# Kernel tuning notes

Hardware: AMD Instinct MI355X
Metric: run time of the kernel (lower is better)

The kernel has to match this reference:

```python
import jax, jax.numpy as jnp
import numpy as np

D, N, F_IN, F_OUT = 2, 4096, 128, 128
DENSITY = 0.005  # avg degree ~20 per row in the 0/1 attention graphs
NEG_INF = -1e30


def setup_inputs() -> dict:
    key = jax.random.key(0)
    ks = jax.random.split(key, 12)
    X = jax.random.normal(ks[0], (D, N, F_IN), dtype=jnp.float32)
    # Dense Laplacian operator used in torch.sparse.mm(L[i], h_p); scaled so tanh stays non-degenerate
    L = jax.random.normal(ks[1], (D, N, N), dtype=jnp.float32) / np.float32(np.sqrt(N))
    # Upper/lower adjacency: 0/1 matrices (GATLayer extracts edges via adj == 1)
    L_u = (jax.random.uniform(ks[2], (D, N, N)) < DENSITY).astype(jnp.float32)
    L_d = (jax.random.uniform(ks[3], (D, N, N)) < DENSITY).astype(jnp.float32)
    s = np.float32(0.05)
    Wp = jax.random.normal(ks[4], (D, F_IN, F_OUT), dtype=jnp.float32) * s
    Ws = jax.random.normal(ks[5], (D, F_IN, F_OUT), dtype=jnp.float32) * s
    Wu = jax.random.normal(ks[6], (D, F_IN, F_OUT), dtype=jnp.float32) * s
    au1 = jax.random.normal(ks[7], (D, F_OUT), dtype=jnp.float32) * s
    au2 = jax.random.normal(ks[8], (D, F_OUT), dtype=jnp.float32) * s
    Wd = jax.random.normal(ks[9], (D, F_IN, F_OUT), dtype=jnp.float32) * s
    ad1 = jax.random.normal(ks[10], (D, F_OUT), dtype=jnp.float32) * s
    ad2 = jax.random.normal(ks[11], (D, F_OUT), dtype=jnp.float32) * s
    return {"X": X, "L": L, "L_u": L_u, "L_d": L_d,
            "Wp": Wp, "Ws": Ws, "Wu": Wu, "au1": au1, "au2": au2,
            "Wd": Wd, "ad1": ad1, "ad2": ad2, "dimensions": D}


def _gat(x, adj, W, a1, a2):
    # GATLayer.forward with boundary=False: linear -> edge scores -> LeakyReLU ->
    # row-wise softmax restricted to adj==1 entries -> sparse mm.
    h = x @ W                                   # [N, F_OUT]
    s1 = h @ a1                                 # [N]  (a_1 linear, bias=False)
    s2 = h @ a2                                 # [N]
    scores = jax.nn.leaky_relu(s1[:, None] + s2[None, :])  # [N, N], slope 0.01
    mask = adj == 1.0
    scores = jnp.where(mask, scores, NEG_INF)
    attn = jax.nn.softmax(scores, axis=1)
    attn = jnp.where(mask, attn, 0.0)           # zero rows with no edges (sparse softmax semantics)
    return attn @ h                             # [N, F_OUT]


def _san_dim(x, L, Lu, Ld, Wp, Ws, Wu, au1, au2, Wd, ad1, ad2):
    h_p = jnp.tanh(L @ (x @ Wp))
    h_s = jnp.tanh(x @ Ws)
    h_u = jnp.tanh(_gat(x, Lu, Wu, au1, au2))
    h_d = jnp.tanh(_gat(x, Ld, Wd, ad1, ad2))
    return h_s + h_u + h_d + h_p


def reference(X, L, L_u, L_d, Wp, Ws, Wu, au1, au2, Wd, ad1, ad2, dimensions):
    # vmap over the `dimensions` simplex levels (all per-level params stacked on axis 0)
    return jax.vmap(_san_dim)(X, L, L_u, L_d, Wp, Ws, Wu, au1, au2, Wd, ad1, ad2)
```

## Files before the change

### kernel.cpp

```cpp
#include <hip/hip_runtime.h>
#include <hip/hip_bf16.h>

#define NN 4096
#define FD 128
#define NDIM 2
#define CAP 256

#define OFF_HMAT 0
#define OFF_SVEC 3145728
#define OFF_HP   3178496
#define OFF_GU   7372800
#define OFF_GD   8421376
#define OFF_H0T  9469952

typedef _Float16 f16x8 __attribute__((ext_vector_type(8)));
typedef float f32x4 __attribute__((ext_vector_type(4)));

union P4 { _Float16 h[4]; int2 i2; };

__device__ __forceinline__ float f4get(const float4& v, int j) {
    return j == 0 ? v.x : j == 1 ? v.y : j == 2 ? v.z : v.w;
}

__global__ __launch_bounds__(256) void k_xw(
    const float* __restrict__ X, const float* __restrict__ Wp,
    const float* __restrict__ Wsm, const float* __restrict__ Wu,
    const float* __restrict__ Wd, float* __restrict__ hmat,
    _Float16* __restrict__ h0T) {
  int d = blockIdx.z, p = blockIdx.y;
  int r0 = blockIdx.x * 128;
  const float* W = (p == 0 ? Wp : p == 1 ? Wsm : p == 2 ? Wu : Wd) + (size_t)d * FD * FD;
  const float* Xd = X + ((size_t)d * NN + r0) * FD;
  __shared__ int4 As4[2048];
  __shared__ int4 Bs4[2048];
  char* As = (char*)As4; char* Bs = (char*)Bs4;
  int t = threadIdx.x;

#pragma unroll 4
  for (int u = 0; u < 16; u++) {
    int id = t + u * 256;
    int row = id >> 5, k4 = (id & 31) * 4;
    float4 v = *(const float4*)(Xd + (size_t)row * FD + k4);
    P4 pk;
    pk.h[0] = (_Float16)v.x; pk.h[1] = (_Float16)v.y;
    pk.h[2] = (_Float16)v.z; pk.h[3] = (_Float16)v.w;
    int off = (row * 256 + k4 * 2) ^ ((row & 7) << 4);
    *(int2*)(As + off) = pk.i2;
  }
#pragma unroll 4
  for (int u = 0; u < 16; u++) {
    int id = t + u * 256;
    int k = id >> 5, n4 = (id & 31) * 4;
    float4 v = *(const float4*)(W + (size_t)k * FD + n4);
#pragma unroll
    for (int j = 0; j < 4; j++) {
      int n = n4 + j;
      int off = (n * 256 + k * 2) ^ ((n & 7) << 4);
      *(_Float16*)(Bs + off) = (_Float16)f4get(v, j);
    }
  }
  __syncthreads();

  int w = t >> 6, l = t & 63;
  int lr = l & 15, lkb = (l >> 4) * 16;
  f32x4 acc[2][8] = {};
#pragma unroll
  for (int kb = 0; kb < 4; kb++) {
    f16x8 a[2], b[8];
#pragma unroll
    for (int m = 0; m < 2; m++) {
      int row = w * 32 + m * 16 + lr;
      int off = (row * 256 + kb * 64 + lkb) ^ ((row & 7) << 4);
      a[m] = *(const f16x8*)(As + off);
    }
#pragma unroll
    for (int n = 0; n < 8; n++) {
      int rn = n * 16 + lr;
      int off = (rn * 256 + kb * 64 + lkb) ^ ((rn & 7) << 4);
      b[n] = *(const f16x8*)(Bs + off);
    }
#pragma unroll
    for (int m = 0; m < 2; m++)
#pragma unroll
      for (int n = 0; n < 8; n++)
        acc[m][n] = __builtin_amdgcn_mfma_f32_16x16x32_f16(a[m], b[n], acc[m][n], 0, 0, 0);
  }

  if (p == 0) {
    _Float16* hT = h0T + (size_t)d * FD * NN;
#pragma unroll
    for (int m = 0; m < 2; m++)
#pragma unroll
      for (int n = 0; n < 8; n++) {
        int col = n * 16 + lr;
        int grow = r0 + w * 32 + m * 16 + (l >> 4) * 4;
        P4 pk;
#pragma unroll
        for (int r = 0; r < 4; r++) pk.h[r] = (_Float16)acc[m][n][r];
        *(int2*)(hT + (size_t)col * NN + grow) = pk.i2;
      }
  } else {
    float* o = hmat + ((size_t)(d * 3 + p - 1) * NN + r0) * FD;
#pragma unroll
    for (int m = 0; m < 2; m++)
#pragma unroll
      for (int n = 0; n < 8; n++)
#pragma unroll
        for (int r = 0; r < 4; r++)
          o[(size_t)(w * 32 + m * 16 + (l >> 4) * 4 + r) * FD + n * 16 + lr] = acc[m][n][r];
  }
}

__global__ __launch_bounds__(256) void k_svec(
    const float* __restrict__ hmat, const float* __restrict__ au1,
    const float* __restrict__ au2, const float* __restrict__ ad1,
    const float* __restrict__ ad2, float* __restrict__ svec) {
  int v = blockIdx.y, d = blockIdx.z;
  int w = threadIdx.x >> 6, lane = threadIdx.x & 63;
  int i = blockIdx.x * 4 + w;
  const float* a = (v == 0 ? au1 : v == 1 ? au2 : v == 2 ? ad1 : ad2) + (size_t)d * FD;
  const float* h = hmat + ((size_t)(d * 3 + 1 + (v >> 1)) * NN + i) * FD;
  float x = h[lane] * a[lane] + h[64 + lane] * a[64 + lane];
#pragma unroll
  for (int o = 1; o < 64; o <<= 1) x += __shfl_xor(x, o);
  if (lane == 0) svec[(size_t)(d * 4 + v) * NN + i] = x;
}

__global__ __launch_bounds__(256) void k_lgemm(
    const float* __restrict__ L, const _Float16* __restrict__ h0T,
    float* __restrict__ hp) {
  int d = blockIdx.z, ks = blockIdx.y;
  int r0 = blockIdx.x * 64;
  const float* Lr = L + (size_t)d * NN * NN;
  const _Float16* hT = h0T + (size_t)d * FD * NN;
  __shared__ int4 As4[512];
  __shared__ int4 Bs4[1024];
  char* As = (char*)As4; char* Bs = (char*)Bs4;
  int t = threadIdx.x;
  int w = t >> 6, l = t & 63;
  int lr = l & 15, lkb = (l >> 4) * 16;
  f32x4 acc[8] = {};
  int kbeg = ks * 1024;
  for (int kk = kbeg; kk < kbeg + 1024; kk += 64) {
#pragma unroll
    for (int u = 0; u < 4; u++) {
      int id = t + u * 256;
      int row = id >> 4, k4 = (id & 15) * 4;
      float4 v = *(const float4*)(Lr + (size_t)(r0 + row) * NN + kk + k4);
      P4 pk;
      pk.h[0] = (_Float16)v.x; pk.h[1] = (_Float16)v.y;
      pk.h[2] = (_Float16)v.z; pk.h[3] = (_Float16)v.w;
      int off = (row * 128 + k4 * 2) ^ ((row & 7) << 4);
      *(int2*)(As + off) = pk.i2;
    }
#pragma unroll
    for (int u = 0; u < 4; u++) {
      int id = t + u * 256;
      int n = id >> 3, k8 = (id & 7) * 8;
      int4 v = *(const int4*)(hT + (size_t)n * NN + kk + k8);
      int off = (n * 128 + k8 * 2) ^ ((n & 7) << 4);
      *(int4*)(Bs + off) = v;
    }
    __syncthreads();
#pragma unroll
    for (int kb = 0; kb < 2; kb++) {
      int row = w * 16 + lr;
      int offA = (row * 128 + kb * 64 + lkb) ^ ((row & 7) << 4);
      f16x8 a = *(const f16x8*)(As + offA);
      f16x8 b[8];
#pragma unroll
      for (int n = 0; n < 8; n++) {
        int rn = n * 16 + lr;
        int off = (rn * 128 + kb * 64 + lkb) ^ ((rn & 7) << 4);
        b[n] = *(const f16x8*)(Bs + off);
      }
#pragma unroll
      for (int n = 0; n < 8; n++)
        acc[n] = __builtin_amdgcn_mfma_f32_16x16x32_f16(a, b[n], acc[n], 0, 0, 0);
    }
    __syncthreads();
  }
  float* o = hp + ((size_t)(d * 4 + ks) * NN + r0) * FD;
#pragma unroll
  for (int n = 0; n < 8; n++)
#pragma unroll
    for (int r = 0; r < 4; r++)
      o[(size_t)(w * 16 + (l >> 4) * 4 + r) * FD + n * 16 + lr] = acc[n][r];
}

__global__ __launch_bounds__(256) void k_gat(
    const float* __restrict__ Lu, const float* __restrict__ Ldn,
    const float* __restrict__ hmat, const float* __restrict__ svec,
    float* __restrict__ gu, float* __restrict__ gd) {
  int d = blockIdx.z, a = blockIdx.y;
  int w = threadIdx.x >> 6, lane = threadIdx.x & 63;
  int i = blockIdx.x * 4 + w;
  const float* Arow = (a ? Ldn : Lu) + ((size_t)d * NN + i) * (size_t)NN;
  const float* h = hmat + (size_t)(d * 3 + 1 + a) * NN * FD;
  const float* s1 = svec + (size_t)(d * 4 + 2 * a) * NN;
  const float* s2 = svec + (size_t)(d * 4 + 2 * a + 1) * NN;
  float* g = (a ? gd : gu) + ((size_t)d * NN + i) * FD;

  __shared__ int ej[4][CAP];
  __shared__ float wt[4][CAP];
  int cnt = 0;
  for (int base = 0; base < NN; base += 1024) {
    float4 v[4];
#pragma unroll
    for (int j = 0; j < 4; j++)
      v[j] = *(const float4*)(Arow + base + j * 256 + lane * 4);
#pragma unroll
    for (int j = 0; j < 4; j++) {
#pragma unroll
      for (int q = 0; q < 4; q++) {
        float vv = f4get(v[j], q);
        unsigned long long m = __ballot(vv == 1.0f);
        if (m) {
          if (vv == 1.0f) {
            int pos = cnt + __popcll(m & ((1ull << lane) - 1ull));
            if (pos < CAP) ej[w][pos] = base + j * 256 + lane * 4 + q;
          }
          cnt += __popcll(m);
        }
      }
    }
  }
  cnt = min(cnt, CAP);
  float s1i = s1[i];
  float mx = -1e30f;
  for (int e0 = 0; e0 < cnt; e0 += 64) {
    int e = e0 + lane;
    float sc = -1e30f;
    if (e < cnt) {
      int j = ej[w][e];
      float x = s1i + s2[j];
      sc = x > 0.0f ? x : 0.01f * x;
      wt[w][e] = sc;
    }
    mx = fmaxf(mx, sc);
  }
#pragma unroll
  for (int o = 1; o < 64; o <<= 1) mx = fmaxf(mx, __shfl_xor(mx, o));
  float sum = 0.0f;
  for (int e0 = 0; e0 < cnt; e0 += 64) {
    int e = e0 + lane;
    float pv = 0.0f;
    if (e < cnt) {
      pv = expf(wt[w][e] - mx);
      wt[w][e] = pv;
    }
    sum += pv;
  }
#pragma unroll
  for (int o = 1; o < 64; o <<= 1) sum += __shfl_xor(sum, o);
  float inv = (cnt > 0) ? 1.0f / sum : 0.0f;
  float acc0 = 0.0f, acc1 = 0.0f;
  int e = 0;
  for (; e + 4 <= cnt; e += 4) {
    const float* r0 = h + (size_t)ej[w][e + 0] * FD;
    const float* r1 = h + (size_t)ej[w][e + 1] * FD;
    const float* r2 = h + (size_t)ej[w][e + 2] * FD;
    const float* r3 = h + (size_t)ej[w][e + 3] * FD;
    float w0 = wt[w][e + 0] * inv, w1 = wt[w][e + 1] * inv;
    float w2 = wt[w][e + 2] * inv, w3 = wt[w][e + 3] * inv;
    float a0 = r0[lane], b0 = r0[64 + lane];
    float a1 = r1[lane], b1 = r1[64 + lane];
    float a2 = r2[lane], b2 = r2[64 + lane];
    float a3 = r3[lane], b3 = r3[64 + lane];
    acc0 += w0 * a0 + w1 * a1 + w2 * a2 + w3 * a3;
    acc1 += w0 * b0 + w1 * b1 + w2 * b2 + w3 * b3;
  }
  for (; e < cnt; e++) {
    float wg = wt[w][e] * inv;
    const float* hr = h + (size_t)ej[w][e] * FD;
    acc0 += wg * hr[lane];
    acc1 += wg * hr[64 + lane];
  }
  g[lane] = acc0;
  g[64 + lane] = acc1;
}

__global__ __launch_bounds__(256) void k_combine(
    const float* __restrict__ hmat, const float* __restrict__ hp,
    const float* __restrict__ gu, const float* __restrict__ gd,
    float* __restrict__ out) {
  const size_t tot4 = (size_t)NDIM * NN * FD / 4;
  for (size_t i4 = (size_t)blockIdx.x * blockDim.x + threadIdx.x; i4 < tot4;
       i4 += (size_t)gridDim.x * blockDim.x) {
    size_t i = i4 * 4;
    int d = (int)(i >> 19);
    size_t rem = i & 524287;
    float4 hs = *(const float4*)(hmat + ((size_t)(d * 3) << 19) + rem);
    float4 p0 = *(const float4*)(hp + ((size_t)(d * 4 + 0) << 19) + rem);
    float4 p1 = *(const float4*)(hp + ((size_t)(d * 4 + 1) << 19) + rem);
    float4 p2 = *(const float4*)(hp + ((size_t)(d * 4 + 2) << 19) + rem);
    float4 p3 = *(const float4*)(hp + ((size_t)(d * 4 + 3) << 19) + rem);
    float4 u = *(const float4*)(gu + ((size_t)d << 19) + rem);
    float4 dd = *(const float4*)(gd + ((size_t)d << 19) + rem);
    float4 o;
    o.x = tanhf(hs.x) + tanhf(u.x) + tanhf(dd.x) + tanhf(p0.x + p1.x + p2.x + p3.x);
    o.y = tanhf(hs.y) + tanhf(u.y) + tanhf(dd.y) + tanhf(p0.y + p1.y + p2.y + p3.y);
    o.z = tanhf(hs.z) + tanhf(u.z) + tanhf(dd.z) + tanhf(p0.z + p1.z + p2.z + p3.z);
    o.w = tanhf(hs.w) + tanhf(u.w) + tanhf(dd.w) + tanhf(p0.w + p1.w + p2.w + p3.w);
    *(float4*)(out + i) = o;
  }
}

extern "C" void kernel_launch(void* const* d_in, const int* in_sizes, int n_in,
                              void* d_out, int out_size, void* d_ws, size_t ws_size,
                              hipStream_t stream) {
  const float* X   = (const float*)d_in[0];
  const float* L   = (const float*)d_in[1];
  const float* Lu  = (const float*)d_in[2];
  const float* Ldn = (const float*)d_in[3];
  const float* Wp  = (const float*)d_in[4];
  const float* Wsm = (const float*)d_in[5];
  const float* Wu  = (const float*)d_in[6];
  const float* au1 = (const float*)d_in[7];
  const float* au2 = (const float*)d_in[8];
  const float* Wd  = (const float*)d_in[9];
  const float* ad1 = (const float*)d_in[10];
  const float* ad2 = (const float*)d_in[11];
  float* out = (float*)d_out;
  float* ws = (float*)d_ws;

  float* hmat = ws + OFF_HMAT;
  float* svec = ws + OFF_SVEC;
  float* hp   = ws + OFF_HP;
  float* gu   = ws + OFF_GU;
  float* gd   = ws + OFF_GD;
  _Float16* h0T = (_Float16*)(ws + OFF_H0T);

  k_xw<<<dim3(NN / 128, 4, NDIM), 256, 0, stream>>>(X, Wp, Wsm, Wu, Wd, hmat, h0T);
  k_svec<<<dim3(NN / 4, 4, NDIM), 256, 0, stream>>>(hmat, au1, au2, ad1, ad2, svec);
  k_lgemm<<<dim3(NN / 64, 4, NDIM), 256, 0, stream>>>(L, h0T, hp);
  k_gat<<<dim3(NN / 4, 2, NDIM), 256, 0, stream>>>(Lu, Ldn, hmat, svec, gu, gd);
  k_combine<<<1024, 256, 0, stream>>>(hmat, hp, gu, gd, out);
}
```

Measured before the change: 128.9 us.

## Process each GAT row with a full block instead of one wave

The GAT kernel now gives each adjacency row a whole 256-thread block instead of a single wave. The four waves scan quarters of the row with ballot compaction and merge their edge lists through shared memory. One wave then computes the softmax, and all threads gather the neighbour features by column, with a final two-way reduction. This aims to spread the latency-bound row scan and gather across more threads, at the cost of extra block syncs, 4x more blocks, and a 64-edge cap per wave quarter.

After: 130.8 us. About the same (+1.4%).

```diff
diff --git a/kernel.cpp b/kernel.cpp
--- a/kernel.cpp
+++ b/kernel.cpp
@@ -188,96 +188,97 @@
       o[(size_t)(w * 16 + (l >> 4) * 4 + r) * FD + n * 16 + lr] = acc[n][r];
 }
 
+#define BAL(val, idxexpr)                                          \
+  {                                                                \
+    unsigned long long m = __ballot((val) == 1.0f);                \
+    if (m) {                                                       \
+      if ((val) == 1.0f) {                                         \
+        int pos = c + __popcll(m & ((1ull << lane) - 1ull));       \
+        if (pos < 64) ejt[w][pos] = (idxexpr);                     \
+      }                                                            \
+      c += __popcll(m);                                            \
+    }                                                              \
+  }
+
 __global__ __launch_bounds__(256) void k_gat(
     const float* __restrict__ Lu, const float* __restrict__ Ldn,
     const float* __restrict__ hmat, const float* __restrict__ svec,
     float* __restrict__ gu, float* __restrict__ gd) {
-  int d = blockIdx.z, a = blockIdx.y;
-  int w = threadIdx.x >> 6, lane = threadIdx.x & 63;
-  int i = blockIdx.x * 4 + w;
+  int i = blockIdx.x;
+  int a = blockIdx.y, d = blockIdx.z;
   const float* Arow = (a ? Ldn : Lu) + ((size_t)d * NN + i) * (size_t)NN;
   const float* h = hmat + (size_t)(d * 3 + 1 + a) * NN * FD;
   const float* s1 = svec + (size_t)(d * 4 + 2 * a) * NN;
   const float* s2 = svec + (size_t)(d * 4 + 2 * a + 1) * NN;
   float* g = (a ? gd : gu) + ((size_t)d * NN + i) * FD;
 
-  __shared__ int ej[4][CAP];
-  __shared__ float wt[4][CAP];
-  int cnt = 0;
-  for (int base = 0; base < NN; base += 1024) {
-    float4 v[4];
-#pragma unroll
-    for (int j = 0; j < 4; j++)
-      v[j] = *(const float4*)(Arow + base + j * 256 + lane * 4);
-#pragma unroll
-    for (int j = 0; j < 4; j++) {
-#pragma unroll
-      for (int q = 0; q < 4; q++) {
-        float vv = f4get(v[j], q);
-        unsigned long long m = __ballot(vv == 1.0f);
-        if (m) {
-          if (vv == 1.0f) {
-            int pos = cnt + __popcll(m & ((1ull << lane) - 1ull));
-            if (pos < CAP) ej[w][pos] = base + j * 256 + lane * 4 + q;
-          }
-          cnt += __popcll(m);
-        }
-      }
-    }
-  }
-  cnt = min(cnt, CAP);
-  float s1i = s1[i];
-  float mx = -1e30f;
-  for (int e0 = 0; e0 < cnt; e0 += 64) {
-    int e = e0 + lane;
-    float sc = -1e30f;
-    if (e < cnt) {
-      int j = ej[w][e];
-      float x = s1i + s2[j];
-      sc = x > 0.0f ? x : 0.01f * x;
-      wt[w][e] = sc;
-    }
-    mx = fmaxf(mx, sc);
-  }
-#pragma unroll
-  for (int o = 1; o < 64; o <<= 1) mx = fmaxf(mx, __shfl_xor(mx, o));
-  float sum = 0.0f;
-  for (int e0 = 0; e0 < cnt; e0 += 64) {
-    int e = e0 + lane;
-    float pv = 0.0f;
-    if (e < cnt) {
-      pv = expf(wt[w][e] - mx);
-      wt[w][e] = pv;
-    }
-    sum += pv;
-  }
-#pragma unroll
-  for (int o = 1; o < 64; o <<= 1) sum += __shfl_xor(sum, o);
-  float inv = (cnt > 0) ? 1.0f / sum : 0.0f;
-  float acc0 = 0.0f, acc1 = 0.0f;
-  int e = 0;
-  for (; e + 4 <= cnt; e += 4) {
-    const float* r0 = h + (size_t)ej[w][e + 0] * FD;
-    const float* r1 = h + (size_t)ej[w][e + 1] * FD;
-    const float* r2 = h + (size_t)ej[w][e + 2] * FD;
-    const float* r3 = h + (size_t)ej[w][e + 3] * FD;
-    float w0 = wt[w][e + 0] * inv, w1 = wt[w][e + 1] * inv;
-    float w2 = wt[w][e + 2] * inv, w3 = wt[w][e + 3] * inv;
-    float a0 = r0[lane], b0 = r0[64 + lane];
-    float a1 = r1[lane], b1 = r1[64 + lane];
-    float a2 = r2[lane], b2 = r2[64 + lane];
-    float a3 = r3[lane], b3 = r3[64 + lane];
-    acc0 += w0 * a0 + w1 * a1 + w2 * a2 + w3 * a3;
-    acc1 += w0 * b0 + w1 * b1 + w2 * b2 + w3 * b3;
-  }
-  for (; e < cnt; e++) {
-    float wg = wt[w][e] * inv;
-    const float* hr = h + (size_t)ej[w][e] * FD;
-    acc0 += wg * hr[lane];
-    acc1 += wg * hr[64 + lane];
-  }
-  g[lane] = acc0;
-  g[64 + lane] = acc1;
+  __shared__ int ejt[4][64];
+  __shared__ int wcnt[4];
+  __shared__ int ejs[CAP];
+  __shared__ float wts[CAP];
+  __shared__ float red[256];
+  __shared__ float invs;
+
+  int t = threadIdx.x, w = t >> 6, lane = t & 63;
+
+  int bi = t * 16;
+  float4 v0 = *(const float4*)(Arow + bi);
+  float4 v1 = *(const float4*)(Arow + bi + 4);
+  float4 v2 = *(const float4*)(Arow + bi + 8);
+  float4 v3 = *(const float4*)(Arow + bi + 12);
+  int c = 0;
+  BAL(v0.x, bi + 0)  BAL(v0.y, bi + 1)  BAL(v0.z, bi + 2)  BAL(v0.w, bi + 3)
+  BAL(v1.x, bi + 4)  BAL(v1.y, bi + 5)  BAL(v1.z, bi + 6)  BAL(v1.w, bi + 7)
+  BAL(v2.x, bi + 8)  BAL(v2.y, bi + 9)  BAL(v2.z, bi + 10) BAL(v2.w, bi + 11)
+  BAL(v3.x, bi + 12) BAL(v3.y, bi + 13) BAL(v3.z, bi + 14) BAL(v3.w, bi + 15)
+  if (lane == 0) wcnt[w] = min(c, 64);
+  __syncthreads();
+
+  int c0 = wcnt[0], c1 = wcnt[1], c2 = wcnt[2], c3 = wcnt[3];
+  int base = (w > 0 ? c0 : 0) + (w > 1 ? c1 : 0) + (w > 2 ? c2 : 0);
+  int cnt = c0 + c1 + c2 + c3;
+  int myc = wcnt[w];
+  if (lane < myc) ejs[base + lane] = ejt[w][lane];
+  __syncthreads();
+
+  if (w == 0) {
+    float s1i = s1[i];
+    float sc0 = -1e30f, sc1 = -1e30f, sc2 = -1e30f, sc3 = -1e30f;
+    if (lane < cnt)       { float x = s1i + s2[ejs[lane]];       sc0 = x > 0.f ? x : 0.01f * x; }
+    if (64 + lane < cnt)  { float x = s1i + s2[ejs[64 + lane]];  sc1 = x > 0.f ? x : 0.01f * x; }
+    if (128 + lane < cnt) { float x = s1i + s2[ejs[128 + lane]]; sc2 = x > 0.f ? x : 0.01f * x; }
+    if (192 + lane < cnt) { float x = s1i + s2[ejs[192 + lane]]; sc3 = x > 0.f ? x : 0.01f * x; }
+    float mx = fmaxf(fmaxf(sc0, sc1), fmaxf(sc2, sc3));
+#pragma unroll
+    for (int o = 1; o < 64; o <<= 1) mx = fmaxf(mx, __shfl_xor(mx, o));
+    float p0 = 0.f, p1 = 0.f, p2 = 0.f, p3 = 0.f;
+    if (lane < cnt)       { p0 = expf(sc0 - mx); wts[lane] = p0; }
+    if (64 + lane < cnt)  { p1 = expf(sc1 - mx); wts[64 + lane] = p1; }
+    if (128 + lane < cnt) { p2 = expf(sc2 - mx); wts[128 + lane] = p2; }
+    if (192 + lane < cnt) { p3 = expf(sc3 - mx); wts[192 + lane] = p3; }
+    float sum = p0 + p1 + p2 + p3;
+#pragma unroll
+    for (int o = 1; o < 64; o <<= 1) sum += __shfl_xor(sum, o);
+    if (lane == 0) invs = (cnt > 0) ? 1.0f / sum : 0.0f;
+  }
+  __syncthreads();
+
+  int col = t & 127;
+  float acc = 0.0f;
+  int e = t >> 7;
+  for (; e + 6 < cnt; e += 8) {
+    int j0 = ejs[e], j1 = ejs[e + 2], j2 = ejs[e + 4], j3 = ejs[e + 6];
+    float w0 = wts[e], w1 = wts[e + 2], w2 = wts[e + 4], w3 = wts[e + 6];
+    float h0 = h[(size_t)j0 * FD + col];
+    float h1 = h[(size_t)j1 * FD + col];
+    float h2 = h[(size_t)j2 * FD + col];
+    float h3 = h[(size_t)j3 * FD + col];
+    acc += w0 * h0 + w1 * h1 + w2 * h2 + w3 * h3;
+  }
+  for (; e < cnt; e += 2) acc += wts[e] * h[(size_t)ejs[e] * FD + col];
+  red[t] = acc * invs;
+  __syncthreads();
+  if (t < 128) g[t] = red[t] + red[t + 128];
 }
 
 __global__ __launch_bounds__(256) void k_combine(
@@ -334,6 +335,6 @@
   k_xw<<<dim3(NN / 128, 4, NDIM), 256, 0, stream>>>(X, Wp, Wsm, Wu, Wd, hmat, h0T);
   k_svec<<<dim3(NN / 4, 4, NDIM), 256, 0, stream>>>(hmat, au1, au2, ad1, ad2, svec);
   k_lgemm<<<dim3(NN / 64, 4, NDIM), 256, 0, stream>>>(L, h0T, hp);
-  k_gat<<<dim3(NN / 4, 2, NDIM), 256, 0, stream>>>(Lu, Ldn, hmat, svec, gu, gd);
+  k_gat<<<dim3(NN, 2, NDIM), 256, 0, stream>>>(Lu, Ldn, hmat, svec, gu, gd);
   k_combine<<<1024, 256, 0, stream>>>(hmat, hp, gu, gd, out);
 }
```

## Replace sparse edge-list GAT with dense masked MFMA attention GEMM

Applied to the files above, without the earlier changes.

The GAT kernel now builds unnormalized exp attention weights densely for 32-row tiles, packs them to fp16 in shared memory, and multiplies them by a transposed fp16 copy of h using MFMA. The row-sum denominator comes from an extra MFMA against a ones vector. The xw kernel now also writes transposed fp16 copies of the Wu and Wd projections. This removes the per-row ballot compaction, the capped edge list and the scattered row gathers, at the cost of dense FLOPs over all N columns, fp16 precision for the weights, and skipping the max-subtraction, so large scores risk fp16 overflow.

Result: slower. 243.4 us (+88.8%).

```diff
diff --git a/kernel.cpp b/kernel.cpp
--- a/kernel.cpp
+++ b/kernel.cpp
@@ -4,7 +4,6 @@
 #define NN 4096
 #define FD 128
 #define NDIM 2
-#define CAP 256
 
 #define OFF_HMAT 0
 #define OFF_SVEC 3145728
@@ -12,6 +11,8 @@
 #define OFF_GU   7372800
 #define OFF_GD   8421376
 #define OFF_H0T  9469952
+#define OFF_HUT  9994240
+#define OFF_HDT  10518528
 
 typedef _Float16 f16x8 __attribute__((ext_vector_type(8)));
 typedef float f32x4 __attribute__((ext_vector_type(4)));
@@ -26,7 +27,8 @@
     const float* __restrict__ X, const float* __restrict__ Wp,
     const float* __restrict__ Wsm, const float* __restrict__ Wu,
     const float* __restrict__ Wd, float* __restrict__ hmat,
-    _Float16* __restrict__ h0T) {
+    _Float16* __restrict__ h0T, _Float16* __restrict__ huT,
+    _Float16* __restrict__ hdT) {
   int d = blockIdx.z, p = blockIdx.y;
   int r0 = blockIdx.x * 128;
   const float* W = (p == 0 ? Wp : p == 1 ? Wsm : p == 2 ? Wu : Wd) + (size_t)d * FD * FD;
@@ -86,8 +88,8 @@
         acc[m][n] = __builtin_amdgcn_mfma_f32_16x16x32_f16(a[m], b[n], acc[m][n], 0, 0, 0);
   }
 
-  if (p == 0) {
-    _Float16* hT = h0T + (size_t)d * FD * NN;
+  if (p != 1) {
+    _Float16* hT = (p == 0 ? h0T : p == 2 ? huT : hdT) + (size_t)d * FD * NN;
 #pragma unroll
     for (int m = 0; m < 2; m++)
 #pragma unroll
@@ -99,7 +101,8 @@
         for (int r = 0; r < 4; r++) pk.h[r] = (_Float16)acc[m][n][r];
         *(int2*)(hT + (size_t)col * NN + grow) = pk.i2;
       }
-  } else {
+  }
+  if (p != 0) {
     float* o = hmat + ((size_t)(d * 3 + p - 1) * NN + r0) * FD;
 #pragma unroll
     for (int m = 0; m < 2; m++)
@@ -188,96 +191,101 @@
       o[(size_t)(w * 16 + (l >> 4) * 4 + r) * FD + n * 16 + lr] = acc[n][r];
 }
 
-__global__ __launch_bounds__(256) void k_gat(
+__global__ __launch_bounds__(256) void k_fgat(
     const float* __restrict__ Lu, const float* __restrict__ Ldn,
-    const float* __restrict__ hmat, const float* __restrict__ svec,
+    const _Float16* __restrict__ huT, const _Float16* __restrict__ hdT,
+    const float* __restrict__ svec,
     float* __restrict__ gu, float* __restrict__ gd) {
-  int d = blockIdx.z, a = blockIdx.y;
-  int w = threadIdx.x >> 6, lane = threadIdx.x & 63;
-  int i = blockIdx.x * 4 + w;
-  const float* Arow = (a ? Ldn : Lu) + ((size_t)d * NN + i) * (size_t)NN;
-  const float* h = hmat + (size_t)(d * 3 + 1 + a) * NN * FD;
+  int r0 = blockIdx.x * 32;
+  int a = blockIdx.y, d = blockIdx.z;
+  const float* A = (a ? Ldn : Lu) + (size_t)d * NN * NN;
+  const _Float16* hT = (a ? hdT : huT) + (size_t)d * FD * NN;
   const float* s1 = svec + (size_t)(d * 4 + 2 * a) * NN;
   const float* s2 = svec + (size_t)(d * 4 + 2 * a + 1) * NN;
-  float* g = (a ? gd : gu) + ((size_t)d * NN + i) * FD;
-
-  __shared__ int ej[4][CAP];
-  __shared__ float wt[4][CAP];
-  int cnt = 0;
-  for (int base = 0; base < NN; base += 1024) {
-    float4 v[4];
-#pragma unroll
-    for (int j = 0; j < 4; j++)
-      v[j] = *(const float4*)(Arow + base + j * 256 + lane * 4);
-#pragma unroll
-    for (int j = 0; j < 4; j++) {
+  float* g = (a ? gd : gu) + ((size_t)d * NN + r0) * FD;
+
+  __shared__ char Ps[32 * 128];
+  __shared__ char Bs[128 * 128];
+
+  int t = threadIdx.x, w = t >> 6, l = t & 63;
+  int wm = w >> 1, wn = w & 1;
+  int lr = l & 15, lkb = (l >> 4) * 16;
+
+  int row = t >> 4, j4 = (t & 15) * 4;
+  int n0 = t >> 3, k8 = (t & 7) * 8;
+  const float* pA0 = A + (size_t)(r0 + row) * NN + j4;
+  const float* pA1 = pA0 + (size_t)16 * NN;
+  const float* pS = s2 + j4;
+  const _Float16* pB0 = hT + (size_t)n0 * NN + k8;
+  int offP0 = (row * 128 + j4 * 2) ^ ((row & 7) << 4);
+  int offB0 = (n0 * 128 + k8 * 2) ^ ((n0 & 7) << 4);
+  float s1a = s1[r0 + row];
+  float s1b = s1[r0 + 16 + row];
+
+  f16x8 ones = {(_Float16)1.f, (_Float16)1.f, (_Float16)1.f, (_Float16)1.f,
+                (_Float16)1.f, (_Float16)1.f, (_Float16)1.f, (_Float16)1.f};
+  f32x4 acc[4] = {};
+  f32x4 dacc = {};
+
+  float4 av0 = *(const float4*)(pA0);
+  float4 av1 = *(const float4*)(pA1);
+  float4 sv  = *(const float4*)(pS);
+  int4 bv[4];
+#pragma unroll
+  for (int u = 0; u < 4; u++) bv[u] = *(const int4*)(pB0 + (size_t)(32 * u) * NN);
+
+  for (int jb = 0; jb < NN; jb += 64) {
+    {
+      P4 pk0, pk1;
 #pragma unroll
       for (int q = 0; q < 4; q++) {
-        float vv = f4get(v[j], q);
-        unsigned long long m = __ballot(vv == 1.0f);
-        if (m) {
-          if (vv == 1.0f) {
-            int pos = cnt + __popcll(m & ((1ull << lane) - 1ull));
-            if (pos < CAP) ej[w][pos] = base + j * 256 + lane * 4 + q;
-          }
-          cnt += __popcll(m);
-        }
+        float sc0 = s1a + f4get(sv, q);
+        sc0 = sc0 > 0.f ? sc0 : 0.01f * sc0;
+        pk0.h[q] = (_Float16)((f4get(av0, q) == 1.0f) ? __expf(sc0) : 0.0f);
+        float sc1 = s1b + f4get(sv, q);
+        sc1 = sc1 > 0.f ? sc1 : 0.01f * sc1;
+        pk1.h[q] = (_Float16)((f4get(av1, q) == 1.0f) ? __expf(sc1) : 0.0f);
       }
-    }
-  }
-  cnt = min(cnt, CAP);
-  float s1i = s1[i];
-  float mx = -1e30f;
-  for (int e0 = 0; e0 < cnt; e0 += 64) {
-    int e = e0 + lane;
-    float sc = -1e30f;
-    if (e < cnt) {
-      int j = ej[w][e];
-      float x = s1i + s2[j];
-      sc = x > 0.0f ? x : 0.01f * x;
-      wt[w][e] = sc;
-    }
-    mx = fmaxf(mx, sc);
-  }
-#pragma unroll
-  for (int o = 1; o < 64; o <<= 1) mx = fmaxf(mx, __shfl_xor(mx, o));
-  float sum = 0.0f;
-  for (int e0 = 0; e0 < cnt; e0 += 64) {
-    int e = e0 + lane;
-    float pv = 0.0f;
-    if (e < cnt) {
-      pv = expf(wt[w][e] - mx);
-      wt[w][e] = pv;
-    }
-    sum += pv;
-  }
-#pragma unroll
-  for (int o = 1; o < 64; o <<= 1) sum += __shfl_xor(sum, o);
-  float inv = (cnt > 0) ? 1.0f / sum : 0.0f;
-  float acc0 = 0.0f, acc1 = 0.0f;
-  int e = 0;
-  for (; e + 4 <= cnt; e += 4) {
-    const float* r0 = h + (size_t)ej[w][e + 0] * FD;
-    const float* r1 = h + (size_t)ej[w][e + 1] * FD;
-    const float* r2 = h + (size_t)ej[w][e + 2] * FD;
-    const float* r3 = h + (size_t)ej[w][e + 3] * FD;
-    float w0 = wt[w][e + 0] * inv, w1 = wt[w][e + 1] * inv;
-    float w2 = wt[w][e + 2] * inv, w3 = wt[w][e + 3] * inv;
-    float a0 = r0[lane], b0 = r0[64 + lane];
-    float a1 = r1[lane], b1 = r1[64 + lane];
-    float a2 = r2[lane], b2 = r2[64 + lane];
-    float a3 = r3[lane], b3 = r3[64 + lane];
-    acc0 += w0 * a0 + w1 * a1 + w2 * a2 + w3 * a3;
-    acc1 += w0 * b0 + w1 * b1 + w2 * b2 + w3 * b3;
-  }
-  for (; e < cnt; e++) {
-    float wg = wt[w][e] * inv;
-    const float* hr = h + (size_t)ej[w][e] * FD;
-    acc0 += wg * hr[lane];
-    acc1 += wg * hr[64 + lane];
-  }
-  g[lane] = acc0;
-  g[64 + lane] = acc1;
+      *(int2*)(Ps + offP0) = pk0.i2;
+      *(int2*)(Ps + offP0 + 2048) = pk1.i2;
+#pragma unroll
+      for (int u = 0; u < 4; u++) *(int4*)(Bs + offB0 + u * 4096) = bv[u];
+    }
+    if (jb + 64 < NN) {
+      av0 = *(const float4*)(pA0 + jb + 64);
+      av1 = *(const float4*)(pA1 + jb + 64);
+      sv  = *(const float4*)(pS + jb + 64);
+#pragma unroll
+      for (int u = 0; u < 4; u++)
+        bv[u] = *(const int4*)(pB0 + (size_t)(32 * u) * NN + jb + 64);
+    }
+    __syncthreads();
+#pragma unroll
+    for (int kb = 0; kb < 2; kb++) {
+      int prow = wm * 16 + lr;
+      int offA = (prow * 128 + kb * 64 + lkb) ^ ((prow & 7) << 4);
+      f16x8 pa = *(const f16x8*)(Ps + offA);
+      dacc = __builtin_amdgcn_mfma_f32_16x16x32_f16(pa, ones, dacc, 0, 0, 0);
+#pragma unroll
+      for (int n = 0; n < 4; n++) {
+        int col = wn * 64 + n * 16 + lr;
+        int offB = (col * 128 + kb * 64 + lkb) ^ ((col & 7) << 4);
+        f16x8 bb = *(const f16x8*)(Bs + offB);
+        acc[n] = __builtin_amdgcn_mfma_f32_16x16x32_f16(pa, bb, acc[n], 0, 0, 0);
+      }
+    }
+    __syncthreads();
+  }
+
+#pragma unroll
+  for (int r = 0; r < 4; r++) {
+    int orow = wm * 16 + (l >> 4) * 4 + r;
+    float den = dacc[r];
+    float inv = den > 0.0f ? 1.0f / den : 0.0f;
+#pragma unroll
+    for (int n = 0; n < 4; n++)
+      g[(size_t)orow * FD + wn * 64 + n * 16 + lr] = acc[n][r] * inv;
+  }
 }
 
 __global__ __launch_bounds__(256) void k_combine(
@@ -330,10 +338,13 @@
   float* gu   = ws + OFF_GU;
   float* gd   = ws + OFF_GD;
   _Float16* h0T = (_Float16*)(ws + OFF_H0T);
-
-  k_xw<<<dim3(NN / 128, 4, NDIM), 256, 0, stream>>>(X, Wp, Wsm, Wu, Wd, hmat, h0T);
+  _Float16* huT = (_Float16*)(ws + OFF_HUT);
+  _Float16* hdT = (_Float16*)(ws + OFF_HDT);
+
+  k_xw<<<dim3(NN / 128, 4, NDIM), 256, 0, stream>>>(X, Wp, Wsm, Wu, Wd, hmat,
+                                                    h0T, huT, hdT);
   k_svec<<<dim3(NN / 4, 4, NDIM), 256, 0, stream>>>(hmat, au1, au2, ad1, ad2, svec);
   k_lgemm<<<dim3(NN / 64, 4, NDIM), 256, 0, stream>>>(L, h0T, hp);
-  k_gat<<<dim3(NN / 4, 2, NDIM), 256, 0, stream>>>(Lu, Ldn, hmat, svec, gu, gd);
+  k_fgat<<<dim3(NN / 32, 2, NDIM), 256, 0, stream>>>(Lu, Ldn, huT, hdT, svec, gu, gd);
   k_combine<<<1024, 256, 0, stream>>>(hmat, hp, gu, gd, out);
 }
```

## Pack adjacency matrices into bitmasks in a separate kernel before GAT

Applied to the files above, without the earlier changes.

Adds a k_pack kernel that streams the dense 0/1 adjacency matrices once and writes per-row 64x64-bit ballot masks to workspace. The GAT kernel then reads one 512-byte mask per row and builds its edge list with a popcount prefix scan plus bit iteration, instead of scanning 4096 floats with 16 serialized ballots per chunk. The dense adjacency is still read in full, so total traffic stays about the same. The gain depends on k_pack being more bandwidth-efficient than the old per-wave scan. It costs an extra launch and a mask write/read round trip.

Result: slower. 141.8 us (+10.0%).

```diff
diff --git a/kernel.cpp b/kernel.cpp
--- a/kernel.cpp
+++ b/kernel.cpp
@@ -5,6 +5,8 @@
 #define FD 128
 #define NDIM 2
 #define CAP 256
+
+typedef unsigned long long u64;
 
 #define OFF_HMAT 0
 #define OFF_SVEC 3145728
@@ -12,6 +14,7 @@
 #define OFF_GU   7372800
 #define OFF_GD   8421376
 #define OFF_H0T  9469952
+#define OFF_MASK 9994240
 
 typedef _Float16 f16x8 __attribute__((ext_vector_type(8)));
 typedef float f32x4 __attribute__((ext_vector_type(4)));
@@ -188,14 +191,48 @@
       o[(size_t)(w * 16 + (l >> 4) * 4 + r) * FD + n * 16 + lr] = acc[n][r];
 }
 
-__global__ __launch_bounds__(256) void k_gat(
+__global__ __launch_bounds__(256) void k_pack(
     const float* __restrict__ Lu, const float* __restrict__ Ldn,
-    const float* __restrict__ hmat, const float* __restrict__ svec,
-    float* __restrict__ gu, float* __restrict__ gd) {
+    u64* __restrict__ mask) {
+  int lane = threadIdx.x & 63;
+  int wid = (blockIdx.x * 256 + threadIdx.x) >> 6;
+  int nw = (gridDim.x * 256) >> 6;
+  const int TOT = 4 * NN * 8;
+  for (int pair = wid; pair < TOT; pair += nw) {
+    int p = pair >> 15;
+    int rg = pair & 32767;
+    int row = rg >> 3, g2 = rg & 7;
+    const float* src = ((p & 1) ? Ldn : Lu) +
+                       ((size_t)(p >> 1) * NN + row) * (size_t)NN + g2 * 512;
+    float4 v0 = *(const float4*)(src + 4 * lane);
+    float4 v1 = *(const float4*)(src + 256 + 4 * lane);
+    u64 m0 = __ballot(v0.x == 1.0f);
+    u64 m1 = __ballot(v0.y == 1.0f);
+    u64 m2 = __ballot(v0.z == 1.0f);
+    u64 m3 = __ballot(v0.w == 1.0f);
+    u64 m4 = __ballot(v1.x == 1.0f);
+    u64 m5 = __ballot(v1.y == 1.0f);
+    u64 m6 = __ballot(v1.z == 1.0f);
+    u64 m7 = __ballot(v1.w == 1.0f);
+    if (lane == 0) {
+      u64* o = mask + ((size_t)p * NN + row) * 64 + g2 * 8;
+      ulonglong2 a0 = {m0, m1}, a1 = {m2, m3}, a2 = {m4, m5}, a3 = {m6, m7};
+      *(ulonglong2*)(o + 0) = a0;
+      *(ulonglong2*)(o + 2) = a1;
+      *(ulonglong2*)(o + 4) = a2;
+      *(ulonglong2*)(o + 6) = a3;
+    }
+  }
+}
+
+__global__ __launch_bounds__(256) void k_gat2(
+    const u64* __restrict__ mask, const float* __restrict__ hmat,
+    const float* __restrict__ svec, float* __restrict__ gu,
+    float* __restrict__ gd) {
   int d = blockIdx.z, a = blockIdx.y;
   int w = threadIdx.x >> 6, lane = threadIdx.x & 63;
   int i = blockIdx.x * 4 + w;
-  const float* Arow = (a ? Ldn : Lu) + ((size_t)d * NN + i) * (size_t)NN;
+  const u64* mrow = mask + ((size_t)((d * 2 + a) * NN) + i) * 64;
   const float* h = hmat + (size_t)(d * 3 + 1 + a) * NN * FD;
   const float* s1 = svec + (size_t)(d * 4 + 2 * a) * NN;
   const float* s2 = svec + (size_t)(d * 4 + 2 * a + 1) * NN;
@@ -203,29 +240,26 @@
 
   __shared__ int ej[4][CAP];
   __shared__ float wt[4][CAP];
-  int cnt = 0;
-  for (int base = 0; base < NN; base += 1024) {
-    float4 v[4];
-#pragma unroll
-    for (int j = 0; j < 4; j++)
-      v[j] = *(const float4*)(Arow + base + j * 256 + lane * 4);
-#pragma unroll
-    for (int j = 0; j < 4; j++) {
-#pragma unroll
-      for (int q = 0; q < 4; q++) {
-        float vv = f4get(v[j], q);
-        unsigned long long m = __ballot(vv == 1.0f);
-        if (m) {
-          if (vv == 1.0f) {
-            int pos = cnt + __popcll(m & ((1ull << lane) - 1ull));
-            if (pos < CAP) ej[w][pos] = base + j * 256 + lane * 4 + q;
-          }
-          cnt += __popcll(m);
-        }
-      }
-    }
+
+  u64 m = mrow[lane];
+  int c = __popcll(m);
+  int pre = c;
+#pragma unroll
+  for (int o = 1; o < 64; o <<= 1) {
+    int tv = __shfl_up(pre, o);
+    if (lane >= o) pre += tv;
+  }
+  int cnt = __shfl(pre, 63);
+  int base = pre - c;
+  int colbase = (lane >> 2) * 256 + (lane & 3);
+  while (m) {
+    int b = __ffsll((unsigned long long)m) - 1;
+    m &= m - 1;
+    if (base < CAP) ej[w][base] = colbase + b * 4;
+    base++;
   }
   cnt = min(cnt, CAP);
+
   float s1i = s1[i];
   float mx = -1e30f;
   for (int e0 = 0; e0 < cnt; e0 += 64) {
@@ -254,6 +288,7 @@
 #pragma unroll
   for (int o = 1; o < 64; o <<= 1) sum += __shfl_xor(sum, o);
   float inv = (cnt > 0) ? 1.0f / sum : 0.0f;
+
   float acc0 = 0.0f, acc1 = 0.0f;
   int e = 0;
   for (; e + 4 <= cnt; e += 4) {
@@ -330,10 +365,12 @@
   float* gu   = ws + OFF_GU;
   float* gd   = ws + OFF_GD;
   _Float16* h0T = (_Float16*)(ws + OFF_H0T);
+  u64* mask = (u64*)(ws + OFF_MASK);
 
   k_xw<<<dim3(NN / 128, 4, NDIM), 256, 0, stream>>>(X, Wp, Wsm, Wu, Wd, hmat, h0T);
   k_svec<<<dim3(NN / 4, 4, NDIM), 256, 0, stream>>>(hmat, au1, au2, ad1, ad2, svec);
+  k_pack<<<2048, 256, 0, stream>>>(Lu, Ldn, mask);
   k_lgemm<<<dim3(NN / 64, 4, NDIM), 256, 0, stream>>>(L, h0T, hp);
-  k_gat<<<dim3(NN / 4, 2, NDIM), 256, 0, stream>>>(Lu, Ldn, hmat, svec, gu, gd);
+  k_gat2<<<dim3(NN / 4, 2, NDIM), 256, 0, stream>>>(mask, hmat, svec, gu, gd);
   k_combine<<<1024, 256, 0, stream>>>(hmat, hp, gu, gd, out);
 }
```
